# Kernel optimization log

Measured on AMD Instinct MI355X. Metric: run time of the kernel, lower is better.

The kernel has to match this reference:

```python
import jax, jax.numpy as jnp
import numpy as np

B, T, D_MODEL, D_HEAD = 4, 2048, 1024, 64

def setup_inputs() -> dict:
    key = jax.random.key(0)
    k1, k2, k3, k4 = jax.random.split(key, 4)
    x = jax.random.normal(k1, (B, T, D_MODEL), dtype=jnp.float32)
    # Linear(d_model, d_head) weights stored as [d_model, d_head] for x @ W
    s = 1.0 / np.sqrt(D_MODEL)
    W_Q = jax.random.normal(k2, (D_MODEL, D_HEAD), dtype=jnp.float32) * s
    W_K = jax.random.normal(k3, (D_MODEL, D_HEAD), dtype=jnp.float32) * s
    W_V = jax.random.normal(k4, (D_MODEL, D_HEAD), dtype=jnp.float32) * s
    return {"x": x, "W_Q": W_Q, "W_K": W_K, "W_V": W_V}

def reference(x, W_Q, W_K, W_V):
    d_head = W_Q.shape[-1]
    Q = jnp.einsum('btm,md->btd', x, W_Q)
    K = jnp.einsum('btm,md->btd', x, W_K)
    V = jnp.einsum('btm,md->btd', x, W_V)
    A = jnp.einsum('bid,bjd->bij', Q, K) / jnp.sqrt(jnp.asarray(d_head, x.dtype))
    T_ = x.shape[1]
    causal = jnp.tril(jnp.ones((T_, T_), dtype=bool))  # [T, T]
    A = jnp.where(causal, A, -jnp.inf)
    A = jax.nn.softmax(A, axis=-1)
    return jnp.einsum('bij,bjd->bid', A, V)
```

## Files before the change

### kernel.cpp

```cpp
#include <hip/hip_runtime.h>
#include <hip/hip_bf16.h>

#define NB 4
#define NT 2048
#define DM 1024
#define DH 64

typedef __attribute__((ext_vector_type(8))) short bf16x8;
typedef __attribute__((ext_vector_type(4))) float f32x4;
typedef unsigned short u16;
typedef unsigned int u32;

static __device__ __forceinline__ u16 f2b(float f) {
    __hip_bfloat16 h = __float2bfloat16(f);
    return __builtin_bit_cast(u16, h);
}
static __device__ __forceinline__ float b2f(u16 h) {
    return __builtin_bit_cast(float, (u32)h << 16);
}
static __device__ __forceinline__ void gld16(const void* g, void* l) {
    __builtin_amdgcn_global_load_lds((const __attribute__((address_space(1))) void*)g,
                                     (__attribute__((address_space(3))) void*)l, 16, 0, 0);
}
#define BAR() __builtin_amdgcn_s_barrier()
#define SBAR() __builtin_amdgcn_sched_barrier(0)

__global__ __launch_bounds__(256) void wt_conv(
    const float* __restrict__ WQ, const float* __restrict__ WK,
    const float* __restrict__ WV, u16* __restrict__ wt)
{
    __shared__ u16 tl[64][68];
    const int which = blockIdx.y, kt = blockIdx.x;
    const float* W = (which == 0) ? WQ : (which == 1) ? WK : WV;
    #pragma unroll
    for (int i = 0; i < 4; ++i) {
        int r = (threadIdx.x >> 4) + i * 16;
        int c = (threadIdx.x & 15) * 4;
        float4 v = *(const float4*)&W[(size_t)(kt * 64 + r) * DH + c];
        tl[r][c] = f2b(v.x); tl[r][c + 1] = f2b(v.y);
        tl[r][c + 2] = f2b(v.z); tl[r][c + 3] = f2b(v.w);
    }
    __syncthreads();
    int d = threadIdx.x >> 2, kc = (threadIdx.x & 3) * 16;
    u16 buf[16];
    #pragma unroll
    for (int j = 0; j < 16; ++j) buf[j] = tl[kc + j][d];
    u16* dst = wt + which * 65536 + d * 1024 + kt * 64 + kc;
    *(uint4*)dst = *(uint4*)&buf[0];
    *(uint4*)(dst + 8) = *(uint4*)&buf[8];
}

__global__ __launch_bounds__(256) void qkv_gemm(
    const float* __restrict__ x, const u16* __restrict__ wt,
    u16* __restrict__ Qb, u16* __restrict__ Kb, u16* __restrict__ Vt)
{
    __shared__ float xs[2][4096];
    __shared__ u16 wsm[2][4096];
    const int tid = threadIdx.x, lane = tid & 63, w = tid >> 6;
    const int l15 = lane & 15, g = lane >> 4;
    const int row0 = blockIdx.x * 64;
    const int which = blockIdx.y;
    const u16* Wg = wt + which * 65536;

    auto stage = [&](int kt, int bi) {
        #pragma unroll
        for (int i = 0; i < 4; ++i) {
            u32 D = (u32)(w * 4096 + i * 1024 + lane * 16);
            u32 r = D >> 8, c = D & 255;
            u32 cs = c ^ ((r & 7) << 5);
            gld16(x + (size_t)(row0 + r) * DM + kt * 64 + (cs >> 2),
                  (char*)&xs[bi][0] + w * 4096 + i * 1024);
        }
        #pragma unroll
        for (int i = 0; i < 2; ++i) {
            u32 D = (u32)(w * 2048 + i * 1024 + lane * 16);
            u32 r = D >> 7, c = D & 127;
            u32 cs = c ^ ((r & 7) << 4);
            gld16(Wg + (size_t)r * 1024 + kt * 64 + (cs >> 1),
                  (char*)&wsm[bi][0] + w * 2048 + i * 1024);
        }
    };

    f32x4 acc[4];
    #pragma unroll
    for (int i = 0; i < 4; ++i) acc[i] = {0.f, 0.f, 0.f, 0.f};

    stage(0, 0);

    const int arow = w * 16 + l15;
    #pragma unroll
    for (int kt = 0; kt < 16; ++kt) {
        if (kt < 15) {
            stage(kt + 1, (kt + 1) & 1);
            asm volatile("s_waitcnt vmcnt(6)" ::: "memory");
        } else {
            asm volatile("s_waitcnt vmcnt(0)" ::: "memory");
        }
        BAR();
        SBAR();
        const char* xb = (const char*)&xs[kt & 1][0];
        const char* wb = (const char*)&wsm[kt & 1][0];
        #pragma unroll
        for (int ks = 0; ks < 2; ++ks) {
            u32 abase = (u32)(arow * 256 + ks * 128 + g * 32);
            f32x4 a0 = *(const f32x4*)(xb + (abase ^ ((arow & 7) << 5)));
            f32x4 a1 = *(const f32x4*)(xb + ((abase + 16) ^ ((arow & 7) << 5)));
            bf16x8 afrag;
            #pragma unroll
            for (int e = 0; e < 4; ++e) afrag[e] = (short)f2b(a0[e]);
            #pragma unroll
            for (int e = 0; e < 4; ++e) afrag[4 + e] = (short)f2b(a1[e]);
            __builtin_amdgcn_s_setprio(1);
            #pragma unroll
            for (int nt = 0; nt < 4; ++nt) {
                int brow = nt * 16 + l15;
                u32 bb = (u32)(brow * 128 + ks * 64 + g * 16);
                bf16x8 bfrag = *(const bf16x8*)(wb + (bb ^ ((brow & 7) << 4)));
                acc[nt] = __builtin_amdgcn_mfma_f32_16x16x32_bf16(afrag, bfrag, acc[nt], 0, 0, 0);
            }
            __builtin_amdgcn_s_setprio(0);
        }
        BAR();
    }
    #pragma unroll
    for (int nt = 0; nt < 4; ++nt) {
        int dcol = nt * 16 + l15;
        #pragma unroll
        for (int r = 0; r < 4; ++r) {
            int row = row0 + w * 16 + g * 4 + r;
            float v = acc[nt][r];
            if (which == 0)      Qb[(size_t)row * DH + dcol] = f2b(v * 0.125f);
            else if (which == 1) Kb[(size_t)row * DH + dcol] = f2b(v);
            else { int bb2 = row >> 11, t = row & 2047;
                   Vt[(size_t)bb2 * DH * NT + (size_t)dcol * NT + t] = f2b(v); }
        }
    }
}

__global__ __launch_bounds__(256) void attn(
    const u16* __restrict__ Qb, const u16* __restrict__ Kb,
    const u16* __restrict__ Vt, u16* __restrict__ pOt, float* __restrict__ pml,
    int CHUNK, int SLOTS)
{
    __shared__ u16 k_lds[2][4096];
    __shared__ u16 v_lds[2][4096];
    __shared__ f32x4 p_lds[4][128];

    const int tid = threadIdx.x, lane = tid & 63, w = tid >> 6;
    const int l15 = lane & 15, g = lane >> 4;
    const int b = blockIdx.y;

    int flat = blockIdx.x, qb = 0, nc;
    for (;;) { nc = (qb + CHUNK) / CHUNK; if (flat < nc) break; flat -= nc; ++qb; }
    const int chunk = flat;
    const int t0 = chunk * CHUNK;
    const int t1 = min(t0 + CHUNK, qb + 1);
    const int q0 = qb * 64;

    const u16* Qg = Qb + ((size_t)b * NT + q0 + w * 16) * DH;
    const u16* Kg = Kb + (size_t)b * NT * DH;
    const u16* Vg = Vt + (size_t)b * DH * NT;

    auto stage = [&](int t, int bi) {
        const int j0 = t * 64;
        #pragma unroll
        for (int i = 0; i < 2; ++i) {
            u32 D = (u32)(w * 2048 + i * 1024 + lane * 16);
            u32 r = D >> 7, c = D & 127;
            u32 cs = c ^ ((r & 7) << 4);
            gld16(Kg + (size_t)(j0 + r) * DH + (cs >> 1),
                  (char*)&k_lds[bi][0] + w * 2048 + i * 1024);
            gld16(Vg + (size_t)r * NT + j0 + (cs >> 1),
                  (char*)&v_lds[bi][0] + w * 2048 + i * 1024);
        }
    };

    stage(t0, 0);

    bf16x8 qf[2];
    qf[0] = *(const bf16x8*)(Qg + l15 * DH + g * 8);
    qf[1] = *(const bf16x8*)(Qg + l15 * DH + 32 + g * 8);

    float m_run = -INFINITY, l_run = 0.f;
    f32x4 oacc[4];
    #pragma unroll
    for (int nt = 0; nt < 4; ++nt) oacc[nt] = {0.f, 0.f, 0.f, 0.f};

    char* pw = (char*)&p_lds[w][0];
    const int swz = (l15 & 7) << 4;

    for (int t = t0; t < t1; ++t) {
        const int cur = (t - t0) & 1;
        if (t + 1 < t1) {
            stage(t + 1, cur ^ 1);
            asm volatile("s_waitcnt vmcnt(4)" ::: "memory");
        } else {
            asm volatile("s_waitcnt vmcnt(0)" ::: "memory");
        }
        BAR();
        SBAR();
        const char* kb = (const char*)&k_lds[cur][0];
        const char* vb = (const char*)&v_lds[cur][0];

        f32x4 sacc[4];
        #pragma unroll
        for (int nt = 0; nt < 4; ++nt) sacc[nt] = {0.f, 0.f, 0.f, 0.f};
        __builtin_amdgcn_s_setprio(1);
        #pragma unroll
        for (int ks = 0; ks < 2; ++ks) {
            #pragma unroll
            for (int nt = 0; nt < 4; ++nt) {
                int arow = nt * 16 + l15;
                u32 aa = (u32)(arow * 128 + ks * 64 + g * 16);
                bf16x8 kf = *(const bf16x8*)(kb + (aa ^ ((arow & 7) << 4)));
                sacc[nt] = __builtin_amdgcn_mfma_f32_16x16x32_bf16(kf, qf[ks], sacc[nt], 0, 0, 0);
            }
        }
        __builtin_amdgcn_s_setprio(0);
        if (t == qb) {
            const int q_local = w * 16 + l15;
            #pragma unroll
            for (int nt = 0; nt < 4; ++nt)
                #pragma unroll
                for (int r = 0; r < 4; ++r)
                    if (nt * 16 + g * 4 + r > q_local) sacc[nt][r] = -1e30f;
        }
        float mx = -INFINITY;
        #pragma unroll
        for (int nt = 0; nt < 4; ++nt) {
            float a = fmaxf(fmaxf(sacc[nt][0], sacc[nt][1]),
                            fmaxf(sacc[nt][2], sacc[nt][3]));
            mx = fmaxf(mx, a);
        }
        mx = fmaxf(mx, __shfl_xor(mx, 16));
        mx = fmaxf(mx, __shfl_xor(mx, 32));
        const float m_new = fmaxf(m_run, mx);
        const float alpha = __expf(m_run - m_new);
        float p[4][4];
        float ps = 0.f;
        #pragma unroll
        for (int nt = 0; nt < 4; ++nt)
            #pragma unroll
            for (int r = 0; r < 4; ++r) {
                float pv = __expf(sacc[nt][r] - m_new);
                p[nt][r] = pv; ps += pv;
            }
        ps += __shfl_xor(ps, 16);
        ps += __shfl_xor(ps, 32);
        l_run = l_run * alpha + ps;
        m_run = m_new;
        #pragma unroll
        for (int nt = 0; nt < 4; ++nt)
            #pragma unroll
            for (int r = 0; r < 4; ++r) oacc[nt][r] *= alpha;

        #pragma unroll
        for (int nt = 0; nt < 4; ++nt) {
            uint2 pk;
            pk.x = (u32)f2b(p[nt][0]) | ((u32)f2b(p[nt][1]) << 16);
            pk.y = (u32)f2b(p[nt][2]) | ((u32)f2b(p[nt][3]) << 16);
            u32 a = (u32)((l15 * 128 + nt * 32 + g * 8) ^ swz);
            *(uint2*)(pw + a) = pk;
        }
        bf16x8 pb[2];
        #pragma unroll
        for (int ks = 0; ks < 2; ++ks)
            pb[ks] = *(const bf16x8*)(pw + ((u32)(l15 * 128 + ks * 64 + g * 16) ^ swz));

        __builtin_amdgcn_s_setprio(1);
        #pragma unroll
        for (int ks = 0; ks < 2; ++ks) {
            #pragma unroll
            for (int nt = 0; nt < 4; ++nt) {
                int arow = nt * 16 + l15;
                u32 aa = (u32)(arow * 128 + ks * 64 + g * 16);
                bf16x8 vf = *(const bf16x8*)(vb + (aa ^ ((arow & 7) << 4)));
                oacc[nt] = __builtin_amdgcn_mfma_f32_16x16x32_bf16(vf, pb[ks], oacc[nt], 0, 0, 0);
            }
        }
        __builtin_amdgcn_s_setprio(0);
        BAR();
    }

    const int slot = (b * 32 + qb) * SLOTS + chunk;
    u16* Op = pOt + (size_t)slot * 4096;
    #pragma unroll
    for (int nt = 0; nt < 4; ++nt)
        #pragma unroll
        for (int r = 0; r < 4; ++r)
            Op[(nt * 16 + g * 4 + r) * 64 + w * 16 + l15] = f2b(oacc[nt][r]);
    if (g == 0) {
        float* mlp = pml + (size_t)slot * 128;
        mlp[(w * 16 + l15) * 2]     = m_run;
        mlp[(w * 16 + l15) * 2 + 1] = l_run;
    }
}

__global__ __launch_bounds__(256) void merge(
    const u16* __restrict__ pOt, const float* __restrict__ pml,
    float* __restrict__ out, int CHUNK, int SLOTS)
{
    __shared__ float tl[64][65];
    const int bq = blockIdx.x;
    const int b = bq >> 5, qb = bq & 31;
    const int nc = (qb + CHUNK) / CHUNK;
    const int base = bq * SLOTS;
    const int q = threadIdx.x & 63, ds = threadIdx.x >> 6;

    float m = -INFINITY;
    for (int c = 0; c < nc; ++c)
        m = fmaxf(m, pml[(size_t)(base + c) * 128 + q * 2]);
    float lsum = 0.f;
    float acc[16];
    #pragma unroll
    for (int i = 0; i < 16; ++i) acc[i] = 0.f;
    for (int c = 0; c < nc; ++c) {
        const float mc = pml[(size_t)(base + c) * 128 + q * 2];
        const float lc = pml[(size_t)(base + c) * 128 + q * 2 + 1];
        const float wc = __expf(mc - m);
        lsum += wc * lc;
        const u16* Op = pOt + (size_t)(base + c) * 4096;
        #pragma unroll
        for (int i = 0; i < 16; ++i)
            acc[i] += wc * b2f(Op[(ds * 16 + i) * 64 + q]);
    }
    const float inv = 1.f / lsum;
    #pragma unroll
    for (int i = 0; i < 16; ++i) tl[q][ds * 16 + i] = acc[i] * inv;
    __syncthreads();
    const int q2 = threadIdx.x >> 2, dc = threadIdx.x & 3;
    float* orow = out + ((size_t)b * NT + qb * 64 + q2) * 64 + dc * 16;
    #pragma unroll
    for (int j4 = 0; j4 < 4; ++j4) {
        float4 v = { tl[q2][dc * 16 + j4 * 4 + 0], tl[q2][dc * 16 + j4 * 4 + 1],
                     tl[q2][dc * 16 + j4 * 4 + 2], tl[q2][dc * 16 + j4 * 4 + 3] };
        *(float4*)&orow[j4 * 4] = v;
    }
}

extern "C" void kernel_launch(void* const* d_in, const int* in_sizes, int n_in,
                              void* d_out, int out_size, void* d_ws, size_t ws_size,
                              hipStream_t stream) {
    const float* x  = (const float*)d_in[0];
    const float* WQ = (const float*)d_in[1];
    const float* WK = (const float*)d_in[2];
    const float* WV = (const float*)d_in[3];
    float* out = (float*)d_out;

    char* ws = (char*)d_ws;
    u16* Qb = (u16*)ws;
    u16* Kb = (u16*)(ws + 1048576);
    u16* Vt = (u16*)(ws + 2097152);
    u16* Wt = (u16*)(ws + 3145728);
    int CHUNK, SLOTS;
    if (ws_size >= 9830400) { CHUNK = 6;  SLOTS = 6; }
    else                    { CHUNK = 16; SLOTS = 2; }
    u16*   pOt = (u16*)(ws + 3145728);
    float* pml = (float*)(ws + 3145728 + (size_t)NB * 32 * SLOTS * 4096 * 2);

    int gx = 0;
    for (int qb = 0; qb < 32; ++qb) gx += (qb + CHUNK) / CHUNK;

    wt_conv<<<dim3(16, 3), 256, 0, stream>>>(WQ, WK, WV, Wt);
    qkv_gemm<<<dim3(128, 3), 256, 0, stream>>>(x, Wt, Qb, Kb, Vt);
    attn<<<dim3(gx, NB), 256, 0, stream>>>(Qb, Kb, Vt, pOt, pml, CHUNK, SLOTS);
    merge<<<NB * 32, 256, 0, stream>>>(pOt, pml, out, CHUNK, SLOTS);
}
```

Before: 45.62 us.

## Load GEMM and attention operands directly to registers, dropping LDS staging

Both the QKV GEMM and the attention kernel stop staging x/W and K/V tiles through shared memory with async global-to-LDS loads and barriers. Each wave now loads its MFMA fragments straight from global memory into registers: a three-deep register prefetch in the GEMM, and per-iteration loads in attention. The attention split also changes to smaller chunks with more slots when the workspace allows it. This removes barrier and LDS traffic but makes each wave load K/V redundantly from global/L2, adds register pressure, and leaves attention without any prefetch.

Result: slower. 87.09 us (+90.9%).

```diff
diff --git a/kernel.cpp b/kernel.cpp
--- a/kernel.cpp
+++ b/kernel.cpp
@@ -18,12 +18,6 @@
 static __device__ __forceinline__ float b2f(u16 h) {
     return __builtin_bit_cast(float, (u32)h << 16);
 }
-static __device__ __forceinline__ void gld16(const void* g, void* l) {
-    __builtin_amdgcn_global_load_lds((const __attribute__((address_space(1))) void*)g,
-                                     (__attribute__((address_space(3))) void*)l, 16, 0, 0);
-}
-#define BAR() __builtin_amdgcn_s_barrier()
-#define SBAR() __builtin_amdgcn_sched_barrier(0)
 
 __global__ __launch_bounds__(256) void wt_conv(
     const float* __restrict__ WQ, const float* __restrict__ WK,
@@ -54,30 +48,27 @@
     const float* __restrict__ x, const u16* __restrict__ wt,
     u16* __restrict__ Qb, u16* __restrict__ Kb, u16* __restrict__ Vt)
 {
-    __shared__ float xs[2][4096];
-    __shared__ u16 wsm[2][4096];
     const int tid = threadIdx.x, lane = tid & 63, w = tid >> 6;
     const int l15 = lane & 15, g = lane >> 4;
     const int row0 = blockIdx.x * 64;
     const int which = blockIdx.y;
-    const u16* Wg = wt + which * 65536;
-
-    auto stage = [&](int kt, int bi) {
-        #pragma unroll
-        for (int i = 0; i < 4; ++i) {
-            u32 D = (u32)(w * 4096 + i * 1024 + lane * 16);
-            u32 r = D >> 8, c = D & 255;
-            u32 cs = c ^ ((r & 7) << 5);
-            gld16(x + (size_t)(row0 + r) * DM + kt * 64 + (cs >> 2),
-                  (char*)&xs[bi][0] + w * 4096 + i * 1024);
-        }
-        #pragma unroll
-        for (int i = 0; i < 2; ++i) {
-            u32 D = (u32)(w * 2048 + i * 1024 + lane * 16);
-            u32 r = D >> 7, c = D & 127;
-            u32 cs = c ^ ((r & 7) << 4);
-            gld16(Wg + (size_t)r * 1024 + kt * 64 + (cs >> 1),
-                  (char*)&wsm[bi][0] + w * 2048 + i * 1024);
+    const float* xr = x + (size_t)(row0 + w * 16 + l15) * DM + g * 8;
+    const u16* wr_ = wt + which * 65536 + (size_t)l15 * 1024 + g * 8;
+
+    f32x4 ab[3][4];
+    bf16x8 bb[3][8];
+
+    auto lda = [&](int kt, int pb) {
+        const float* xk = xr + kt * 64;
+        ab[pb][0] = *(const f32x4*)(xk);
+        ab[pb][1] = *(const f32x4*)(xk + 4);
+        ab[pb][2] = *(const f32x4*)(xk + 32);
+        ab[pb][3] = *(const f32x4*)(xk + 36);
+        const u16* wk = wr_ + kt * 64;
+        #pragma unroll
+        for (int nt = 0; nt < 4; ++nt) {
+            bb[pb][nt * 2]     = *(const bf16x8*)(wk + nt * 16384);
+            bb[pb][nt * 2 + 1] = *(const bf16x8*)(wk + nt * 16384 + 32);
         }
     };
 
@@ -85,42 +76,28 @@
     #pragma unroll
     for (int i = 0; i < 4; ++i) acc[i] = {0.f, 0.f, 0.f, 0.f};
 
-    stage(0, 0);
-
-    const int arow = w * 16 + l15;
+    lda(0, 0);
+    lda(1, 1);
     #pragma unroll
     for (int kt = 0; kt < 16; ++kt) {
-        if (kt < 15) {
-            stage(kt + 1, (kt + 1) & 1);
-            asm volatile("s_waitcnt vmcnt(6)" ::: "memory");
-        } else {
-            asm volatile("s_waitcnt vmcnt(0)" ::: "memory");
-        }
-        BAR();
-        SBAR();
-        const char* xb = (const char*)&xs[kt & 1][0];
-        const char* wb = (const char*)&wsm[kt & 1][0];
-        #pragma unroll
-        for (int ks = 0; ks < 2; ++ks) {
-            u32 abase = (u32)(arow * 256 + ks * 128 + g * 32);
-            f32x4 a0 = *(const f32x4*)(xb + (abase ^ ((arow & 7) << 5)));
-            f32x4 a1 = *(const f32x4*)(xb + ((abase + 16) ^ ((arow & 7) << 5)));
-            bf16x8 afrag;
-            #pragma unroll
-            for (int e = 0; e < 4; ++e) afrag[e] = (short)f2b(a0[e]);
-            #pragma unroll
-            for (int e = 0; e < 4; ++e) afrag[4 + e] = (short)f2b(a1[e]);
-            __builtin_amdgcn_s_setprio(1);
-            #pragma unroll
-            for (int nt = 0; nt < 4; ++nt) {
-                int brow = nt * 16 + l15;
-                u32 bb = (u32)(brow * 128 + ks * 64 + g * 16);
-                bf16x8 bfrag = *(const bf16x8*)(wb + (bb ^ ((brow & 7) << 4)));
-                acc[nt] = __builtin_amdgcn_mfma_f32_16x16x32_bf16(afrag, bfrag, acc[nt], 0, 0, 0);
+        const int pb = kt % 3;
+        if (kt + 2 < 16) lda(kt + 2, (kt + 2) % 3);
+        bf16x8 af[2];
+        #pragma unroll
+        for (int ks = 0; ks < 2; ++ks)
+            #pragma unroll
+            for (int e = 0; e < 4; ++e) {
+                af[ks][e]     = (short)f2b(ab[pb][ks * 2][e]);
+                af[ks][e + 4] = (short)f2b(ab[pb][ks * 2 + 1][e]);
             }
-            __builtin_amdgcn_s_setprio(0);
-        }
-        BAR();
+        __builtin_amdgcn_s_setprio(1);
+        #pragma unroll
+        for (int ks = 0; ks < 2; ++ks)
+            #pragma unroll
+            for (int nt = 0; nt < 4; ++nt)
+                acc[nt] = __builtin_amdgcn_mfma_f32_16x16x32_bf16(
+                    af[ks], bb[pb][nt * 2 + ks], acc[nt], 0, 0, 0);
+        __builtin_amdgcn_s_setprio(0);
     }
     #pragma unroll
     for (int nt = 0; nt < 4; ++nt) {
@@ -142,8 +119,6 @@
     const u16* __restrict__ Vt, u16* __restrict__ pOt, float* __restrict__ pml,
     int CHUNK, int SLOTS)
 {
-    __shared__ u16 k_lds[2][4096];
-    __shared__ u16 v_lds[2][4096];
     __shared__ f32x4 p_lds[4][128];
 
     const int tid = threadIdx.x, lane = tid & 63, w = tid >> 6;
@@ -158,24 +133,8 @@
     const int q0 = qb * 64;
 
     const u16* Qg = Qb + ((size_t)b * NT + q0 + w * 16) * DH;
-    const u16* Kg = Kb + (size_t)b * NT * DH;
-    const u16* Vg = Vt + (size_t)b * DH * NT;
-
-    auto stage = [&](int t, int bi) {
-        const int j0 = t * 64;
-        #pragma unroll
-        for (int i = 0; i < 2; ++i) {
-            u32 D = (u32)(w * 2048 + i * 1024 + lane * 16);
-            u32 r = D >> 7, c = D & 127;
-            u32 cs = c ^ ((r & 7) << 4);
-            gld16(Kg + (size_t)(j0 + r) * DH + (cs >> 1),
-                  (char*)&k_lds[bi][0] + w * 2048 + i * 1024);
-            gld16(Vg + (size_t)r * NT + j0 + (cs >> 1),
-                  (char*)&v_lds[bi][0] + w * 2048 + i * 1024);
-        }
-    };
-
-    stage(t0, 0);
+    const u16* Kg = Kb + (size_t)b * NT * DH + (size_t)l15 * DH + g * 8;
+    const u16* Vg = Vt + (size_t)b * DH * NT + (size_t)l15 * NT + g * 8;
 
     bf16x8 qf[2];
     qf[0] = *(const bf16x8*)(Qg + l15 * DH + g * 8);
@@ -190,32 +149,31 @@
     const int swz = (l15 & 7) << 4;
 
     for (int t = t0; t < t1; ++t) {
-        const int cur = (t - t0) & 1;
-        if (t + 1 < t1) {
-            stage(t + 1, cur ^ 1);
-            asm volatile("s_waitcnt vmcnt(4)" ::: "memory");
-        } else {
-            asm volatile("s_waitcnt vmcnt(0)" ::: "memory");
-        }
-        BAR();
-        SBAR();
-        const char* kb = (const char*)&k_lds[cur][0];
-        const char* vb = (const char*)&v_lds[cur][0];
+        const int j0 = t * 64;
+        const u16* kp = Kg + (size_t)j0 * DH;
+        const u16* vp = Vg + j0;
+        bf16x8 kf[8], vf[8];
+        #pragma unroll
+        for (int nt = 0; nt < 4; ++nt) {
+            kf[nt * 2]     = *(const bf16x8*)(kp + nt * 1024);
+            kf[nt * 2 + 1] = *(const bf16x8*)(kp + nt * 1024 + 32);
+        }
+        #pragma unroll
+        for (int nt = 0; nt < 4; ++nt) {
+            vf[nt * 2]     = *(const bf16x8*)(vp + nt * 16 * NT);
+            vf[nt * 2 + 1] = *(const bf16x8*)(vp + nt * 16 * NT + 32);
+        }
 
         f32x4 sacc[4];
         #pragma unroll
         for (int nt = 0; nt < 4; ++nt) sacc[nt] = {0.f, 0.f, 0.f, 0.f};
         __builtin_amdgcn_s_setprio(1);
         #pragma unroll
-        for (int ks = 0; ks < 2; ++ks) {
-            #pragma unroll
-            for (int nt = 0; nt < 4; ++nt) {
-                int arow = nt * 16 + l15;
-                u32 aa = (u32)(arow * 128 + ks * 64 + g * 16);
-                bf16x8 kf = *(const bf16x8*)(kb + (aa ^ ((arow & 7) << 4)));
-                sacc[nt] = __builtin_amdgcn_mfma_f32_16x16x32_bf16(kf, qf[ks], sacc[nt], 0, 0, 0);
-            }
-        }
+        for (int ks = 0; ks < 2; ++ks)
+            #pragma unroll
+            for (int nt = 0; nt < 4; ++nt)
+                sacc[nt] = __builtin_amdgcn_mfma_f32_16x16x32_bf16(
+                    kf[nt * 2 + ks], qf[ks], sacc[nt], 0, 0, 0);
         __builtin_amdgcn_s_setprio(0);
         if (t == qb) {
             const int q_local = w * 16 + l15;
@@ -262,24 +220,19 @@
             u32 a = (u32)((l15 * 128 + nt * 32 + g * 8) ^ swz);
             *(uint2*)(pw + a) = pk;
         }
-        bf16x8 pb[2];
-        #pragma unroll
-        for (int ks = 0; ks < 2; ++ks)
-            pb[ks] = *(const bf16x8*)(pw + ((u32)(l15 * 128 + ks * 64 + g * 16) ^ swz));
+        bf16x8 pb_[2];
+        #pragma unroll
+        for (int ks = 0; ks < 2; ++ks)
+            pb_[ks] = *(const bf16x8*)(pw + ((u32)(l15 * 128 + ks * 64 + g * 16) ^ swz));
 
         __builtin_amdgcn_s_setprio(1);
         #pragma unroll
-        for (int ks = 0; ks < 2; ++ks) {
-            #pragma unroll
-            for (int nt = 0; nt < 4; ++nt) {
-                int arow = nt * 16 + l15;
-                u32 aa = (u32)(arow * 128 + ks * 64 + g * 16);
-                bf16x8 vf = *(const bf16x8*)(vb + (aa ^ ((arow & 7) << 4)));
-                oacc[nt] = __builtin_amdgcn_mfma_f32_16x16x32_bf16(vf, pb[ks], oacc[nt], 0, 0, 0);
-            }
-        }
+        for (int ks = 0; ks < 2; ++ks)
+            #pragma unroll
+            for (int nt = 0; nt < 4; ++nt)
+                oacc[nt] = __builtin_amdgcn_mfma_f32_16x16x32_bf16(
+                    vf[nt * 2 + ks], pb_[ks], oacc[nt], 0, 0, 0);
         __builtin_amdgcn_s_setprio(0);
-        BAR();
     }
 
     const int slot = (b * 32 + qb) * SLOTS + chunk;
@@ -353,8 +306,8 @@
     u16* Vt = (u16*)(ws + 2097152);
     u16* Wt = (u16*)(ws + 3145728);
     int CHUNK, SLOTS;
-    if (ws_size >= 9830400) { CHUNK = 6;  SLOTS = 6; }
-    else                    { CHUNK = 16; SLOTS = 2; }
+    if (ws_size >= 12058624) { CHUNK = 4;  SLOTS = 8; }
+    else                     { CHUNK = 16; SLOTS = 2; }
     u16*   pOt = (u16*)(ws + 3145728);
     float* pml = (float*)(ws + 3145728 + (size_t)NB * 32 * SLOTS * 4096 * 2);
 
```

## Split attention into fixed two-tile KV chunks with both tiles prefetched upfront

Applied to the files above, without the earlier changes.

Hard-codes the split-KV chunk size to two key tiles per work item, launching 272 attention blocks per batch instead of the earlier ws-size-dependent chunking. Both K/V tiles are issued at kernel start and the loop is fully unrolled, with a trailing barrier removed. The aim is more parallelism and shorter per-block serial chains. The cost is more partial outputs for the merge kernel to read and combine. It also relies on a larger workspace layout with the partials moved to a new offset, and it drops the fallback for small workspaces.

Result: slower. 46.60 us (+2.1%).

```diff
diff --git a/kernel.cpp b/kernel.cpp
--- a/kernel.cpp
+++ b/kernel.cpp
@@ -140,7 +140,7 @@
 __global__ __launch_bounds__(256) void attn(
     const u16* __restrict__ Qb, const u16* __restrict__ Kb,
     const u16* __restrict__ Vt, u16* __restrict__ pOt, float* __restrict__ pml,
-    int CHUNK, int SLOTS)
+    int SLOTS)
 {
     __shared__ u16 k_lds[2][4096];
     __shared__ u16 v_lds[2][4096];
@@ -151,15 +151,19 @@
     const int b = blockIdx.y;
 
     int flat = blockIdx.x, qb = 0, nc;
-    for (;;) { nc = (qb + CHUNK) / CHUNK; if (flat < nc) break; flat -= nc; ++qb; }
+    for (;;) { nc = (qb + 2) >> 1; if (flat < nc) break; flat -= nc; ++qb; }
     const int chunk = flat;
-    const int t0 = chunk * CHUNK;
-    const int t1 = min(t0 + CHUNK, qb + 1);
+    const int t0 = chunk * 2;
+    const int two = (t0 + 1 <= qb);
     const int q0 = qb * 64;
 
     const u16* Qg = Qb + ((size_t)b * NT + q0 + w * 16) * DH;
     const u16* Kg = Kb + (size_t)b * NT * DH;
     const u16* Vg = Vt + (size_t)b * DH * NT;
+
+    bf16x8 qf[2];
+    qf[0] = *(const bf16x8*)(Qg + l15 * DH + g * 8);
+    qf[1] = *(const bf16x8*)(Qg + l15 * DH + 32 + g * 8);
 
     auto stage = [&](int t, int bi) {
         const int j0 = t * 64;
@@ -174,12 +178,8 @@
                   (char*)&v_lds[bi][0] + w * 2048 + i * 1024);
         }
     };
-
     stage(t0, 0);
-
-    bf16x8 qf[2];
-    qf[0] = *(const bf16x8*)(Qg + l15 * DH + g * 8);
-    qf[1] = *(const bf16x8*)(Qg + l15 * DH + 32 + g * 8);
+    if (two) stage(t0 + 1, 1);
 
     float m_run = -INFINITY, l_run = 0.f;
     f32x4 oacc[4];
@@ -189,18 +189,22 @@
     char* pw = (char*)&p_lds[w][0];
     const int swz = (l15 & 7) << 4;
 
-    for (int t = t0; t < t1; ++t) {
-        const int cur = (t - t0) & 1;
-        if (t + 1 < t1) {
-            stage(t + 1, cur ^ 1);
-            asm volatile("s_waitcnt vmcnt(4)" ::: "memory");
-        } else {
+    if (two) asm volatile("s_waitcnt vmcnt(4)" ::: "memory");
+    else     asm volatile("s_waitcnt vmcnt(0)" ::: "memory");
+    BAR();
+    SBAR();
+
+    #pragma unroll
+    for (int ti = 0; ti < 2; ++ti) {
+        if (ti == 1) {
+            if (!two) break;
             asm volatile("s_waitcnt vmcnt(0)" ::: "memory");
-        }
-        BAR();
-        SBAR();
-        const char* kb = (const char*)&k_lds[cur][0];
-        const char* vb = (const char*)&v_lds[cur][0];
+            BAR();
+            SBAR();
+        }
+        const int t = t0 + ti;
+        const char* kb = (const char*)&k_lds[ti][0];
+        const char* vb = (const char*)&v_lds[ti][0];
 
         f32x4 sacc[4];
         #pragma unroll
@@ -262,10 +266,10 @@
             u32 a = (u32)((l15 * 128 + nt * 32 + g * 8) ^ swz);
             *(uint2*)(pw + a) = pk;
         }
-        bf16x8 pb[2];
+        bf16x8 pb_[2];
         #pragma unroll
         for (int ks = 0; ks < 2; ++ks)
-            pb[ks] = *(const bf16x8*)(pw + ((u32)(l15 * 128 + ks * 64 + g * 16) ^ swz));
+            pb_[ks] = *(const bf16x8*)(pw + ((u32)(l15 * 128 + ks * 64 + g * 16) ^ swz));
 
         __builtin_amdgcn_s_setprio(1);
         #pragma unroll
@@ -275,11 +279,10 @@
                 int arow = nt * 16 + l15;
                 u32 aa = (u32)(arow * 128 + ks * 64 + g * 16);
                 bf16x8 vf = *(const bf16x8*)(vb + (aa ^ ((arow & 7) << 4)));
-                oacc[nt] = __builtin_amdgcn_mfma_f32_16x16x32_bf16(vf, pb[ks], oacc[nt], 0, 0, 0);
+                oacc[nt] = __builtin_amdgcn_mfma_f32_16x16x32_bf16(vf, pb_[ks], oacc[nt], 0, 0, 0);
             }
         }
         __builtin_amdgcn_s_setprio(0);
-        BAR();
     }
 
     const int slot = (b * 32 + qb) * SLOTS + chunk;
@@ -298,12 +301,12 @@
 
 __global__ __launch_bounds__(256) void merge(
     const u16* __restrict__ pOt, const float* __restrict__ pml,
-    float* __restrict__ out, int CHUNK, int SLOTS)
+    float* __restrict__ out, int SLOTS)
 {
     __shared__ float tl[64][65];
     const int bq = blockIdx.x;
     const int b = bq >> 5, qb = bq & 31;
-    const int nc = (qb + CHUNK) / CHUNK;
+    const int nc = (qb + 2) >> 1;
     const int base = bq * SLOTS;
     const int q = threadIdx.x & 63, ds = threadIdx.x >> 6;
 
@@ -352,17 +355,12 @@
     u16* Kb = (u16*)(ws + 1048576);
     u16* Vt = (u16*)(ws + 2097152);
     u16* Wt = (u16*)(ws + 3145728);
-    int CHUNK, SLOTS;
-    if (ws_size >= 9830400) { CHUNK = 6;  SLOTS = 6; }
-    else                    { CHUNK = 16; SLOTS = 2; }
-    u16*   pOt = (u16*)(ws + 3145728);
-    float* pml = (float*)(ws + 3145728 + (size_t)NB * 32 * SLOTS * 4096 * 2);
-
-    int gx = 0;
-    for (int qb = 0; qb < 32; ++qb) gx += (qb + CHUNK) / CHUNK;
+    const int SLOTS = 16;
+    u16*   pOt = (u16*)(ws + 3538944);
+    float* pml = (float*)(ws + 3538944 + (size_t)NB * 32 * SLOTS * 4096 * 2);
 
     wt_conv<<<dim3(16, 3), 256, 0, stream>>>(WQ, WK, WV, Wt);
     qkv_gemm<<<dim3(128, 3), 256, 0, stream>>>(x, Wt, Qb, Kb, Vt);
-    attn<<<dim3(gx, NB), 256, 0, stream>>>(Qb, Kb, Vt, pOt, pml, CHUNK, SLOTS);
-    merge<<<NB * 32, 256, 0, stream>>>(pOt, pml, out, CHUNK, SLOTS);
-}
+    attn<<<dim3(272, NB), 256, 0, stream>>>(Qb, Kb, Vt, pOt, pml, SLOTS);
+    merge<<<NB * 32, 256, 0, stream>>>(pOt, pml, out, SLOTS);
+}
```

## Fuse Q/K/V projections into one GEMM pass reading x once

Applied to the files above, without the earlier changes.

Replaces the per-projection GEMM grid (which re-read x three times, once per Q/K/V) with a single kernel where each block computes all 192 output columns for 32 rows. It uses a 32-wide K step with triple-buffered LDS staging. The intent is to cut the fp32 x global traffic threefold and deepen prefetch. It also hardcodes CHUNK/SLOTS to 6 and moves the partial buffers past the weight buffer, which drops the fallback for small workspaces. The grid becomes 256 blocks and the weight B-fragment loads lose their swizzle, which may cause LDS bank conflicts.

New measurement: 51.86 us. 1.14x slower.

```diff
diff --git a/kernel.cpp b/kernel.cpp
--- a/kernel.cpp
+++ b/kernel.cpp
@@ -5,6 +5,8 @@
 #define NT 2048
 #define DM 1024
 #define DH 64
+#define CHUNK 6
+#define SLOTS 6
 
 typedef __attribute__((ext_vector_type(8))) short bf16x8;
 typedef __attribute__((ext_vector_type(4))) float f32x4;
@@ -45,102 +47,110 @@
     u16 buf[16];
     #pragma unroll
     for (int j = 0; j < 16; ++j) buf[j] = tl[kc + j][d];
-    u16* dst = wt + which * 65536 + d * 1024 + kt * 64 + kc;
+    u16* dst = wt + (size_t)(which * 64 + d) * 1024 + kt * 64 + kc;
     *(uint4*)dst = *(uint4*)&buf[0];
     *(uint4*)(dst + 8) = *(uint4*)&buf[8];
 }
 
-__global__ __launch_bounds__(256) void qkv_gemm(
+__global__ __launch_bounds__(256) void qkv3(
     const float* __restrict__ x, const u16* __restrict__ wt,
     u16* __restrict__ Qb, u16* __restrict__ Kb, u16* __restrict__ Vt)
 {
-    __shared__ float xs[2][4096];
-    __shared__ u16 wsm[2][4096];
+    __shared__ float xs[3][1024];
+    __shared__ u16 wsm[3][6144];
     const int tid = threadIdx.x, lane = tid & 63, w = tid >> 6;
     const int l15 = lane & 15, g = lane >> 4;
-    const int row0 = blockIdx.x * 64;
-    const int which = blockIdx.y;
-    const u16* Wg = wt + which * 65536;
-
-    auto stage = [&](int kt, int bi) {
-        #pragma unroll
-        for (int i = 0; i < 4; ++i) {
-            u32 D = (u32)(w * 4096 + i * 1024 + lane * 16);
-            u32 r = D >> 8, c = D & 255;
-            u32 cs = c ^ ((r & 7) << 5);
-            gld16(x + (size_t)(row0 + r) * DM + kt * 64 + (cs >> 2),
-                  (char*)&xs[bi][0] + w * 4096 + i * 1024);
-        }
-        #pragma unroll
-        for (int i = 0; i < 2; ++i) {
-            u32 D = (u32)(w * 2048 + i * 1024 + lane * 16);
+    const int row0 = blockIdx.x * 32;
+
+    auto stage = [&](int s, int bi) {
+        const int kk = s * 32;
+        {
+            u32 D = (u32)(w * 1024 + lane * 16);
             u32 r = D >> 7, c = D & 127;
             u32 cs = c ^ ((r & 7) << 4);
-            gld16(Wg + (size_t)r * 1024 + kt * 64 + (cs >> 1),
-                  (char*)&wsm[bi][0] + w * 2048 + i * 1024);
+            gld16(x + (size_t)(row0 + r) * DM + kk + (cs >> 2),
+                  (char*)&xs[bi][0] + w * 1024);
+        }
+        #pragma unroll
+        for (int i = 0; i < 3; ++i) {
+            u32 D = (u32)(w * 3072 + i * 1024 + lane * 16);
+            u32 r = D >> 6, c = D & 63;
+            gld16(wt + (size_t)r * 1024 + kk + (c >> 1),
+                  (char*)&wsm[bi][0] + w * 3072 + i * 1024);
         }
     };
 
-    f32x4 acc[4];
-    #pragma unroll
-    for (int i = 0; i < 4; ++i) acc[i] = {0.f, 0.f, 0.f, 0.f};
+    f32x4 acc[2][3];
+    #pragma unroll
+    for (int mf = 0; mf < 2; ++mf)
+        #pragma unroll
+        for (int nt = 0; nt < 3; ++nt) acc[mf][nt] = {0.f, 0.f, 0.f, 0.f};
 
     stage(0, 0);
-
-    const int arow = w * 16 + l15;
-    #pragma unroll
-    for (int kt = 0; kt < 16; ++kt) {
-        if (kt < 15) {
-            stage(kt + 1, (kt + 1) & 1);
-            asm volatile("s_waitcnt vmcnt(6)" ::: "memory");
-        } else {
-            asm volatile("s_waitcnt vmcnt(0)" ::: "memory");
-        }
+    stage(1, 1);
+
+    for (int s = 0; s < 32; ++s) {
+        if (s + 2 < 32) stage(s + 2, (s + 2) % 3);
+        if (s < 30)       asm volatile("s_waitcnt vmcnt(8)" ::: "memory");
+        else if (s == 30) asm volatile("s_waitcnt vmcnt(4)" ::: "memory");
+        else              asm volatile("s_waitcnt vmcnt(0)" ::: "memory");
         BAR();
         SBAR();
-        const char* xb = (const char*)&xs[kt & 1][0];
-        const char* wb = (const char*)&wsm[kt & 1][0];
-        #pragma unroll
-        for (int ks = 0; ks < 2; ++ks) {
-            u32 abase = (u32)(arow * 256 + ks * 128 + g * 32);
-            f32x4 a0 = *(const f32x4*)(xb + (abase ^ ((arow & 7) << 5)));
-            f32x4 a1 = *(const f32x4*)(xb + ((abase + 16) ^ ((arow & 7) << 5)));
-            bf16x8 afrag;
-            #pragma unroll
-            for (int e = 0; e < 4; ++e) afrag[e] = (short)f2b(a0[e]);
-            #pragma unroll
-            for (int e = 0; e < 4; ++e) afrag[4 + e] = (short)f2b(a1[e]);
-            __builtin_amdgcn_s_setprio(1);
-            #pragma unroll
-            for (int nt = 0; nt < 4; ++nt) {
-                int brow = nt * 16 + l15;
-                u32 bb = (u32)(brow * 128 + ks * 64 + g * 16);
-                bf16x8 bfrag = *(const bf16x8*)(wb + (bb ^ ((brow & 7) << 4)));
-                acc[nt] = __builtin_amdgcn_mfma_f32_16x16x32_bf16(afrag, bfrag, acc[nt], 0, 0, 0);
+        const char* xb = (const char*)&xs[s % 3][0];
+        const char* wb = (const char*)&wsm[s % 3][0];
+
+        bf16x8 afrag[2];
+        #pragma unroll
+        for (int mf = 0; mf < 2; ++mf) {
+            const int arow = mf * 16 + l15;
+            const u32 sw = (u32)((arow & 7) << 4);
+            u32 ab = (u32)(arow * 128 + g * 32);
+            f32x4 a0 = *(const f32x4*)(xb + (ab ^ sw));
+            f32x4 a1 = *(const f32x4*)(xb + ((ab + 16) ^ sw));
+            #pragma unroll
+            for (int e = 0; e < 4; ++e) afrag[mf][e] = (short)f2b(a0[e]);
+            #pragma unroll
+            for (int e = 0; e < 4; ++e) afrag[mf][4 + e] = (short)f2b(a1[e]);
+        }
+        bf16x8 bfrag[3];
+        #pragma unroll
+        for (int nt = 0; nt < 3; ++nt) {
+            const int dd = w * 48 + nt * 16 + l15;
+            bfrag[nt] = *(const bf16x8*)(wb + dd * 64 + g * 16);
+        }
+        __builtin_amdgcn_s_setprio(1);
+        #pragma unroll
+        for (int mf = 0; mf < 2; ++mf)
+            #pragma unroll
+            for (int nt = 0; nt < 3; ++nt)
+                acc[mf][nt] = __builtin_amdgcn_mfma_f32_16x16x32_bf16(
+                    afrag[mf], bfrag[nt], acc[mf][nt], 0, 0, 0);
+        __builtin_amdgcn_s_setprio(0);
+        BAR();
+    }
+
+    #pragma unroll
+    for (int mf = 0; mf < 2; ++mf) {
+        #pragma unroll
+        for (int nt = 0; nt < 3; ++nt) {
+            const int dcg = w * 48 + nt * 16 + l15;
+            const int which = dcg >> 6, dcol = dcg & 63;
+            #pragma unroll
+            for (int r = 0; r < 4; ++r) {
+                const int row = row0 + mf * 16 + g * 4 + r;
+                const float v = acc[mf][nt][r];
+                if (which == 0)      Qb[(size_t)row * DH + dcol] = f2b(v * 0.125f);
+                else if (which == 1) Kb[(size_t)row * DH + dcol] = f2b(v);
+                else { int bb2 = row >> 11, t = row & 2047;
+                       Vt[(size_t)bb2 * DH * NT + (size_t)dcol * NT + t] = f2b(v); }
             }
-            __builtin_amdgcn_s_setprio(0);
-        }
-        BAR();
-    }
-    #pragma unroll
-    for (int nt = 0; nt < 4; ++nt) {
-        int dcol = nt * 16 + l15;
-        #pragma unroll
-        for (int r = 0; r < 4; ++r) {
-            int row = row0 + w * 16 + g * 4 + r;
-            float v = acc[nt][r];
-            if (which == 0)      Qb[(size_t)row * DH + dcol] = f2b(v * 0.125f);
-            else if (which == 1) Kb[(size_t)row * DH + dcol] = f2b(v);
-            else { int bb2 = row >> 11, t = row & 2047;
-                   Vt[(size_t)bb2 * DH * NT + (size_t)dcol * NT + t] = f2b(v); }
         }
     }
 }
 
 __global__ __launch_bounds__(256) void attn(
     const u16* __restrict__ Qb, const u16* __restrict__ Kb,
-    const u16* __restrict__ Vt, u16* __restrict__ pOt, float* __restrict__ pml,
-    int CHUNK, int SLOTS)
+    const u16* __restrict__ Vt, u16* __restrict__ pOt, float* __restrict__ pml)
 {
     __shared__ u16 k_lds[2][4096];
     __shared__ u16 v_lds[2][4096];
@@ -174,7 +184,6 @@
                   (char*)&v_lds[bi][0] + w * 2048 + i * 1024);
         }
     };
-
     stage(t0, 0);
 
     bf16x8 qf[2];
@@ -262,10 +271,10 @@
             u32 a = (u32)((l15 * 128 + nt * 32 + g * 8) ^ swz);
             *(uint2*)(pw + a) = pk;
         }
-        bf16x8 pb[2];
+        bf16x8 pb_[2];
         #pragma unroll
         for (int ks = 0; ks < 2; ++ks)
-            pb[ks] = *(const bf16x8*)(pw + ((u32)(l15 * 128 + ks * 64 + g * 16) ^ swz));
+            pb_[ks] = *(const bf16x8*)(pw + ((u32)(l15 * 128 + ks * 64 + g * 16) ^ swz));
 
         __builtin_amdgcn_s_setprio(1);
         #pragma unroll
@@ -275,14 +284,14 @@
                 int arow = nt * 16 + l15;
                 u32 aa = (u32)(arow * 128 + ks * 64 + g * 16);
                 bf16x8 vf = *(const bf16x8*)(vb + (aa ^ ((arow & 7) << 4)));
-                oacc[nt] = __builtin_amdgcn_mfma_f32_16x16x32_bf16(vf, pb[ks], oacc[nt], 0, 0, 0);
+                oacc[nt] = __builtin_amdgcn_mfma_f32_16x16x32_bf16(vf, pb_[ks], oacc[nt], 0, 0, 0);
             }
         }
         __builtin_amdgcn_s_setprio(0);
         BAR();
     }
 
-    const int slot = (b * 32 + qb) * SLOTS + chunk;
+    const int slot = ((b * 32 + qb)) * SLOTS + chunk;
     u16* Op = pOt + (size_t)slot * 4096;
     #pragma unroll
     for (int nt = 0; nt < 4; ++nt)
@@ -298,7 +307,7 @@
 
 __global__ __launch_bounds__(256) void merge(
     const u16* __restrict__ pOt, const float* __restrict__ pml,
-    float* __restrict__ out, int CHUNK, int SLOTS)
+    float* __restrict__ out)
 {
     __shared__ float tl[64][65];
     const int bq = blockIdx.x;
@@ -348,21 +357,15 @@
     float* out = (float*)d_out;
 
     char* ws = (char*)d_ws;
-    u16* Qb = (u16*)ws;
-    u16* Kb = (u16*)(ws + 1048576);
-    u16* Vt = (u16*)(ws + 2097152);
-    u16* Wt = (u16*)(ws + 3145728);
-    int CHUNK, SLOTS;
-    if (ws_size >= 9830400) { CHUNK = 6;  SLOTS = 6; }
-    else                    { CHUNK = 16; SLOTS = 2; }
-    u16*   pOt = (u16*)(ws + 3145728);
-    float* pml = (float*)(ws + 3145728 + (size_t)NB * 32 * SLOTS * 4096 * 2);
-
-    int gx = 0;
-    for (int qb = 0; qb < 32; ++qb) gx += (qb + CHUNK) / CHUNK;
+    u16*   Qb  = (u16*)ws;
+    u16*   Kb  = (u16*)(ws + 1048576);
+    u16*   Vt  = (u16*)(ws + 2097152);
+    u16*   Wt  = (u16*)(ws + 3145728);
+    u16*   pOt = (u16*)(ws + 3538944);
+    float* pml = (float*)(ws + 3538944 + 6291456);
 
     wt_conv<<<dim3(16, 3), 256, 0, stream>>>(WQ, WK, WV, Wt);
-    qkv_gemm<<<dim3(128, 3), 256, 0, stream>>>(x, Wt, Qb, Kb, Vt);
-    attn<<<dim3(gx, NB), 256, 0, stream>>>(Qb, Kb, Vt, pOt, pml, CHUNK, SLOTS);
-    merge<<<NB * 32, 256, 0, stream>>>(pOt, pml, out, CHUNK, SLOTS);
-}
+    qkv3<<<256, 256, 0, stream>>>(x, Wt, Qb, Kb, Vt);
+    attn<<<dim3(102, NB), 256, 0, stream>>>(Qb, Kb, Vt, pOt, pml);
+    merge<<<NB * 32, 256, 0, stream>>>(pOt, pml, out);
+}
```
